# Kernel optimization log

Hardware: AMD Instinct MI355X
Metric: run time of the kernel (lower is better)

The kernel has to match this reference:

```python
import jax, jax.numpy as jnp
import numpy as np

N = 100000   # nodes
E = 800000   # edges
H = 256      # hidden_dim == input_dim
L = 3        # num_layers
G = 64       # graphs in batch


def setup_inputs() -> dict:
    key = jax.random.key(0)
    ks = jax.random.split(key, 16)
    s = 0.05
    inp = {
        'x': jax.random.normal(ks[0], (N, H), jnp.float32),
        'edge_index': jax.random.randint(ks[1], (2, E), 0, N, dtype=jnp.int32),
        'batch': jnp.sort(jax.random.randint(ks[2], (N,), 0, G, dtype=jnp.int32)),
        'Ws': jax.random.normal(ks[3], (L, H, H), jnp.float32) * s,
        'Wn': jax.random.normal(ks[4], (L, H, H), jnp.float32) * s,
        'bs': jnp.zeros((L, H), jnp.float32),
        'att_w': jax.random.normal(ks[5], (H, 1), jnp.float32) * s,
        'att_b': jnp.zeros((1,), jnp.float32),
        'ne_W1': jax.random.normal(ks[6], (H, H // 2), jnp.float32) * s,
        'ne_b1': jnp.zeros((H // 2,), jnp.float32),
        'ne_W2': jax.random.normal(ks[7], (H // 2, 1), jnp.float32) * s,
        'ne_b2': jnp.zeros((1,), jnp.float32),
        'nd_W1': jax.random.normal(ks[8], (H, H // 2), jnp.float32) * s,
        'nd_b1': jnp.zeros((H // 2,), jnp.float32),
        'nd_W2': jax.random.normal(ks[9], (H // 2, 1), jnp.float32) * s,
        'nd_b2': jnp.zeros((1,), jnp.float32),
    }
    return inp


def reference(x, edge_index, batch, Ws, Wn, bs, att_w, att_b,
              ne_W1, ne_b1, ne_W2, ne_b2, nd_W1, nd_b1, nd_W2, nd_b2):
    src, dst = edge_index[0], edge_index[1]
    n = x.shape[0]
    # in-degree for mean aggregation (clamped to avoid div-by-zero)
    deg = jax.ops.segment_sum(jnp.ones(src.shape[0], x.dtype), dst, num_segments=n)
    deg = jnp.maximum(deg, 1.0)[:, None]                    # [N,1]
    # GNN encoder: SAGE-mean layers, ReLU (dropout identity at eval)
    h = x
    for l in range(Ws.shape[0]):
        msg = jax.ops.segment_sum(h[src], dst, num_segments=n) / deg  # [N,H]
        h = jax.nn.relu(h @ Ws[l] + msg @ Wn[l] + bs[l])
    # attention pooling: per-graph softmax over node scores
    s = (h @ att_w + att_b)[:, 0]                           # [N]
    m = jax.ops.segment_max(s, batch, num_segments=G)
    e = jnp.exp(s - m[batch])
    denom = jax.ops.segment_sum(e, batch, num_segments=G)
    alpha = (e / denom[batch])[:, None]                     # [N,1]
    g = jax.ops.segment_sum(alpha * h, batch, num_segments=G)  # [G,H]
    # heads: Linear-ReLU-(Dropout)-Linear
    graph_logits = jax.nn.relu(g @ ne_W1 + ne_b1) @ ne_W2 + ne_b2  # [G,1]
    node_logits = jax.nn.relu(h @ nd_W1 + nd_b1) @ nd_W2 + nd_b2  # [N,1]
    return (graph_logits, node_logits)
```

## Files before the change

kernel.cpp:

```cpp
#include <hip/hip_runtime.h>
#include <hip/hip_bf16.h>

#define HID 256
#define HHALF 128

typedef unsigned short u16;
typedef __attribute__((ext_vector_type(8))) short bf16x8;
typedef __attribute__((ext_vector_type(4))) float f32x4;

__device__ __forceinline__ float bf2f(unsigned int u) {
    unsigned int x = (u & 0xffffu) << 16;
    union { unsigned int i; float f; } c; c.i = x; return c.f;
}
__device__ __forceinline__ float lof(unsigned u) {
    union { unsigned i; float f; } c; c.i = u << 16; return c.f;
}
__device__ __forceinline__ float hif(unsigned u) {
    union { unsigned i; float f; } c; c.i = u & 0xffff0000u; return c.f;
}
__device__ __forceinline__ u16 f2bf(float f) {
    __hip_bfloat16 h = __float2bfloat16(f);
    union { __hip_bfloat16 h; u16 u; } c; c.h = h; return c.u;
}

__device__ __forceinline__ void gload16(const u16* g, u16* l) {
    __builtin_amdgcn_global_load_lds(
        (const __attribute__((address_space(1))) void*)g,
        (__attribute__((address_space(3))) void*)l, 16, 0, 0);
}

__global__ void k_count(const int* __restrict__ dst, int* __restrict__ cnt, int E) {
    int i = blockIdx.x * blockDim.x + threadIdx.x;
    if (i < E) atomicAdd(&cnt[dst[i]], 1);
}

__global__ void k_scan_block(const int* __restrict__ cnt, int* __restrict__ bsum, int n) {
    __shared__ int sd[256];
    int tid = threadIdx.x;
    int i = blockIdx.x * 256 + tid;
    int v = (i < n) ? cnt[i] : 0;
    sd[tid] = v; __syncthreads();
    for (int s = 128; s > 0; s >>= 1) {
        if (tid < s) sd[tid] += sd[tid + s];
        __syncthreads();
    }
    if (tid == 0) bsum[blockIdx.x] = sd[0];
}

__global__ void k_scan_top(int* __restrict__ bsum, int nb) {
    __shared__ int sd[512];
    int t = threadIdx.x;
    int v = (t < nb) ? bsum[t] : 0;
    sd[t] = v; __syncthreads();
    for (int s = 1; s < 512; s <<= 1) {
        int x = (t >= s) ? sd[t - s] : 0;
        __syncthreads();
        sd[t] += x;
        __syncthreads();
    }
    if (t < nb) bsum[t] = sd[t] - v;
}

__global__ void k_scan_down(const int* __restrict__ cnt, const int* __restrict__ boff,
                            int* __restrict__ row_off, int n, int total) {
    __shared__ int sd[256];
    int tid = threadIdx.x;
    int i = blockIdx.x * 256 + tid;
    int v = (i < n) ? cnt[i] : 0;
    sd[tid] = v; __syncthreads();
    for (int s = 1; s < 256; s <<= 1) {
        int x = (tid >= s) ? sd[tid - s] : 0;
        __syncthreads();
        sd[tid] += x;
        __syncthreads();
    }
    if (i < n) row_off[i] = boff[blockIdx.x] + sd[tid] - v;
    if (i == 0) row_off[n] = total;
}

__global__ void k_scatter(const int* __restrict__ src, const int* __restrict__ dst,
                          const int* __restrict__ row_off, int* __restrict__ fill,
                          int* __restrict__ col, int E) {
    int i = blockIdx.x * blockDim.x + threadIdx.x;
    if (i < E) {
        int d = dst[i];
        int p = atomicAdd(&fill[d], 1);
        col[row_off[d] + p] = src[i];
    }
}

__global__ void k_f2b(const float* __restrict__ in, u16* __restrict__ o, int total4) {
    int i = blockIdx.x * blockDim.x + threadIdx.x;
    if (i >= total4) return;
    float4 v = *(const float4*)&in[(size_t)i * 4];
    uint2 p;
    p.x = (unsigned)f2bf(v.x) | ((unsigned)f2bf(v.y) << 16);
    p.y = (unsigned)f2bf(v.z) | ((unsigned)f2bf(v.w) << 16);
    *(uint2*)&o[(size_t)i * 4] = p;
}

__global__ void k_wt_all(const float* __restrict__ Ws, const float* __restrict__ Wn,
                         const float* __restrict__ ndW1,
                         u16* __restrict__ WsT, u16* __restrict__ WnT,
                         u16* __restrict__ ndW1T, int L) {
    int idx = blockIdx.x * 256 + threadIdx.x;
    int mat = idx >> 16;
    int r = idx & 65535;
    int k = r >> 8, c = r & 255;
    if (mat < L) {
        WsT[(size_t)mat * 65536 + c * 256 + k] = f2bf(Ws[(size_t)mat * 65536 + k * 256 + c]);
    } else if (mat < 2 * L) {
        int l = mat - L;
        WnT[(size_t)l * 65536 + c * 256 + k] = f2bf(Wn[(size_t)l * 65536 + k * 256 + c]);
    } else {
        if (c < HHALF) ndW1T[c * 256 + k] = f2bf(ndW1[k * HHALF + c]);
    }
}

__global__ __launch_bounds__(256) void k_agg(
    const u16* __restrict__ h, const int* __restrict__ row_off,
    const int* __restrict__ col, u16* __restrict__ msg, int n) {
    int node = blockIdx.x * 4 + (threadIdx.x >> 6);
    if (node >= n) return;
    int lane = threadIdx.x & 63;
    int half = lane >> 5;
    int t = lane & 31;
    int s0 = row_off[node], s1 = row_off[node + 1];
    float a0 = 0.f, a1 = 0.f, a2 = 0.f, a3 = 0.f;
    float a4 = 0.f, a5 = 0.f, a6 = 0.f, a7 = 0.f;
    int e = s0;
    for (; e + 8 <= s1; e += 8) {
        int c0 = col[e + half];
        int c1 = col[e + 2 + half];
        int c2 = col[e + 4 + half];
        int c3 = col[e + 6 + half];
        uint4 v0 = *(const uint4*)&h[(size_t)c0 * HID + t * 8];
        uint4 v1 = *(const uint4*)&h[(size_t)c1 * HID + t * 8];
        uint4 v2 = *(const uint4*)&h[(size_t)c2 * HID + t * 8];
        uint4 v3 = *(const uint4*)&h[(size_t)c3 * HID + t * 8];
        a0 += (lof(v0.x) + lof(v1.x)) + (lof(v2.x) + lof(v3.x));
        a1 += (hif(v0.x) + hif(v1.x)) + (hif(v2.x) + hif(v3.x));
        a2 += (lof(v0.y) + lof(v1.y)) + (lof(v2.y) + lof(v3.y));
        a3 += (hif(v0.y) + hif(v1.y)) + (hif(v2.y) + hif(v3.y));
        a4 += (lof(v0.z) + lof(v1.z)) + (lof(v2.z) + lof(v3.z));
        a5 += (hif(v0.z) + hif(v1.z)) + (hif(v2.z) + hif(v3.z));
        a6 += (lof(v0.w) + lof(v1.w)) + (lof(v2.w) + lof(v3.w));
        a7 += (hif(v0.w) + hif(v1.w)) + (hif(v2.w) + hif(v3.w));
    }
    if (e < s1) {
        int i0 = e + half, i1 = e + 2 + half, i2 = e + 4 + half, i3 = e + 6 + half;
        float w0 = (i0 < s1) ? 1.f : 0.f; int c0 = col[(i0 < s1) ? i0 : s0];
        float w1 = (i1 < s1) ? 1.f : 0.f; int c1 = col[(i1 < s1) ? i1 : s0];
        float w2 = (i2 < s1) ? 1.f : 0.f; int c2 = col[(i2 < s1) ? i2 : s0];
        float w3 = (i3 < s1) ? 1.f : 0.f; int c3 = col[(i3 < s1) ? i3 : s0];
        uint4 v0 = *(const uint4*)&h[(size_t)c0 * HID + t * 8];
        uint4 v1 = *(const uint4*)&h[(size_t)c1 * HID + t * 8];
        uint4 v2 = *(const uint4*)&h[(size_t)c2 * HID + t * 8];
        uint4 v3 = *(const uint4*)&h[(size_t)c3 * HID + t * 8];
        a0 = fmaf(w0, lof(v0.x), fmaf(w1, lof(v1.x), fmaf(w2, lof(v2.x), fmaf(w3, lof(v3.x), a0))));
        a1 = fmaf(w0, hif(v0.x), fmaf(w1, hif(v1.x), fmaf(w2, hif(v2.x), fmaf(w3, hif(v3.x), a1))));
        a2 = fmaf(w0, lof(v0.y), fmaf(w1, lof(v1.y), fmaf(w2, lof(v2.y), fmaf(w3, lof(v3.y), a2))));
        a3 = fmaf(w0, hif(v0.y), fmaf(w1, hif(v1.y), fmaf(w2, hif(v2.y), fmaf(w3, hif(v3.y), a3))));
        a4 = fmaf(w0, lof(v0.z), fmaf(w1, lof(v1.z), fmaf(w2, lof(v2.z), fmaf(w3, lof(v3.z), a4))));
        a5 = fmaf(w0, hif(v0.z), fmaf(w1, hif(v1.z), fmaf(w2, hif(v2.z), fmaf(w3, hif(v3.z), a5))));
        a6 = fmaf(w0, lof(v0.w), fmaf(w1, lof(v1.w), fmaf(w2, lof(v2.w), fmaf(w3, lof(v3.w), a6))));
        a7 = fmaf(w0, hif(v0.w), fmaf(w1, hif(v1.w), fmaf(w2, hif(v2.w), fmaf(w3, hif(v3.w), a7))));
    }
    a0 += __shfl_xor(a0, 32); a1 += __shfl_xor(a1, 32);
    a2 += __shfl_xor(a2, 32); a3 += __shfl_xor(a3, 32);
    a4 += __shfl_xor(a4, 32); a5 += __shfl_xor(a5, 32);
    a6 += __shfl_xor(a6, 32); a7 += __shfl_xor(a7, 32);
    if (half == 0) {
        int deg = s1 - s0;
        float inv = 1.0f / (float)(deg > 1 ? deg : 1);
        uint4 o;
        o.x = (unsigned)f2bf(a0 * inv) | ((unsigned)f2bf(a1 * inv) << 16);
        o.y = (unsigned)f2bf(a2 * inv) | ((unsigned)f2bf(a3 * inv) << 16);
        o.z = (unsigned)f2bf(a4 * inv) | ((unsigned)f2bf(a5 * inv) << 16);
        o.w = (unsigned)f2bf(a6 * inv) | ((unsigned)f2bf(a7 * inv) << 16);
        *(uint4*)&msg[(size_t)node * HID + t * 8] = o;
    }
}

__global__ __launch_bounds__(512) void k_gemm_bf(
    const u16* __restrict__ A1, const u16* __restrict__ W1t,
    const u16* __restrict__ A2, const u16* __restrict__ W2t,
    const float* __restrict__ bias, u16* __restrict__ out,
    int n, int ncols,
    const float* __restrict__ dotw, const float* __restrict__ dotb,
    float* __restrict__ dotout) {
    __shared__ __align__(16) u16 As[128 * 64];
    __shared__ __align__(16) u16 Bs[256 * 64];
    const int tid  = threadIdx.x;
    const int lane = tid & 63;
    const int w    = tid >> 6;
    const int wr   = w >> 2, wc = w & 3;
    const int brow = blockIdx.x * 128;
    const int nkt  = A2 ? 8 : 4;

    f32x4 acc[4][4];
    #pragma unroll
    for (int m = 0; m < 4; ++m)
        #pragma unroll
        for (int q = 0; q < 4; ++q)
            acc[m][q] = (f32x4){0.f, 0.f, 0.f, 0.f};

    const int as0 = tid, as1 = tid + 512;
    int ar0 = brow + (as0 >> 3); if (ar0 >= n) ar0 = n - 1;
    int ar1 = brow + (as1 >> 3); if (ar1 >= n) ar1 = n - 1;
    const size_t asrc0 = (size_t)ar0 * HID + (size_t)(((as0 & 7) ^ (((as0 >> 3) >> 1) & 7)) * 8);
    const size_t asrc1 = (size_t)ar1 * HID + (size_t)(((as1 & 7) ^ (((as1 >> 3) >> 1) & 7)) * 8);
    u16* adst0 = &As[(w * 64) * 8];
    u16* adst1 = &As[(512 + w * 64) * 8];

    size_t bsrc[4];
    u16*   bdst[4];
    #pragma unroll
    for (int i = 0; i < 4; ++i) {
        int s = tid + i * 512;
        int row = s >> 3;
        bsrc[i] = (size_t)row * HID + (size_t)(((s & 7) ^ ((row >> 1) & 7)) * 8);
        bdst[i] = &Bs[(i * 512 + w * 64) * 8];
    }

    const int lr = lane & 15;
    const int lq = lane >> 4;
    const int swz = (lr >> 1) & 7;

    for (int kt = 0; kt < nkt; ++kt) {
        const u16* A = (kt < 4) ? A1 : A2;
        const u16* W = (kt < 4) ? W1t : W2t;
        const int k0 = (kt & 3) * 64;
        __syncthreads();
        gload16(A + asrc0 + k0, adst0);
        gload16(A + asrc1 + k0, adst1);
        gload16(W + bsrc[0] + k0, bdst[0]);
        gload16(W + bsrc[1] + k0, bdst[1]);
        gload16(W + bsrc[2] + k0, bdst[2]);
        gload16(W + bsrc[3] + k0, bdst[3]);
        __syncthreads();
        #pragma unroll
        for (int ks = 0; ks < 2; ++ks) {
            const int ch = (ks * 4 + lq) ^ swz;
            bf16x8 af[4], bg[4];
            #pragma unroll
            for (int m = 0; m < 4; ++m)
                af[m] = *(const bf16x8*)&As[(wr * 64 + m * 16 + lr) * 64 + ch * 8];
            #pragma unroll
            for (int q = 0; q < 4; ++q)
                bg[q] = *(const bf16x8*)&Bs[(wc * 64 + q * 16 + lr) * 64 + ch * 8];
            #pragma unroll
            for (int m = 0; m < 4; ++m)
                #pragma unroll
                for (int q = 0; q < 4; ++q)
                    acc[m][q] = __builtin_amdgcn_mfma_f32_16x16x32_bf16(
                        bg[q], af[m], acc[m][q], 0, 0, 0);
        }
    }

    #pragma unroll
    for (int m = 0; m < 4; ++m) {
        int row = brow + wr * 64 + m * 16 + lr;
        if (row >= n) continue;
        float dpart = 0.f;
        #pragma unroll
        for (int q = 0; q < 4; ++q) {
            int col = wc * 64 + q * 16 + lq * 4;
            if (col < ncols) {
                float4 bb = *(const float4*)&bias[col];
                float r0 = fmaxf(acc[m][q][0] + bb.x, 0.f);
                float r1 = fmaxf(acc[m][q][1] + bb.y, 0.f);
                float r2 = fmaxf(acc[m][q][2] + bb.z, 0.f);
                float r3 = fmaxf(acc[m][q][3] + bb.w, 0.f);
                if (out) {
                    uint2 o;
                    o.x = (unsigned)f2bf(r0) | ((unsigned)f2bf(r1) << 16);
                    o.y = (unsigned)f2bf(r2) | ((unsigned)f2bf(r3) << 16);
                    *(uint2*)&out[(size_t)row * ncols + col] = o;
                }
                if (dotout) {
                    float4 wv = *(const float4*)&dotw[col];
                    dpart += r0 * wv.x + r1 * wv.y + r2 * wv.z + r3 * wv.w;
                }
            }
        }
        if (dotout && (wc * 64 < ncols)) {
            dpart += __shfl_xor(dpart, 16);
            dpart += __shfl_xor(dpart, 32);
            if (lane < 16) {
                float add = dpart + ((wc == 0) ? dotb[0] : 0.f);
                atomicAdd(&dotout[row], add);
            }
        }
    }
}

__global__ void k_gstart(const int* __restrict__ batch, int* __restrict__ gstart, int n, int G) {
    int i = blockIdx.x * blockDim.x + threadIdx.x;
    if (i >= n) return;
    int b = batch[i];
    int bp = (i == 0) ? -1 : batch[i - 1];
    for (int g = bp + 1; g <= b; ++g) gstart[g] = i;
    if (i == n - 1) {
        for (int g = b + 1; g <= G; ++g) gstart[g] = n;
    }
}

__global__ void k_mdenom(const float* __restrict__ s, const int* __restrict__ gstart,
                         float* __restrict__ m, float* __restrict__ denom) {
    int g = blockIdx.x;
    int t = threadIdx.x;
    int i0 = gstart[g], i1 = gstart[g + 1];
    __shared__ float red[256];
    float mx = -INFINITY;
    for (int i = i0 + t; i < i1; i += 256) mx = fmaxf(mx, s[i]);
    red[t] = mx; __syncthreads();
    for (int st = 128; st; st >>= 1) {
        if (t < st) red[t] = fmaxf(red[t], red[t + st]);
        __syncthreads();
    }
    float gm = red[0];
    __syncthreads();
    float sm = 0.f;
    for (int i = i0 + t; i < i1; i += 256) sm += expf(s[i] - gm);
    red[t] = sm; __syncthreads();
    for (int st = 128; st; st >>= 1) {
        if (t < st) red[t] += red[t + st];
        __syncthreads();
    }
    if (t == 0) { m[g] = gm; denom[g] = red[0]; }
}

__global__ void k_pool(const u16* __restrict__ h, const float* __restrict__ sarr,
                       const float* __restrict__ marr, const float* __restrict__ denom,
                       const int* __restrict__ gstart, float* __restrict__ gpool) {
    int g = blockIdx.x, sp = blockIdx.y, t = threadIdx.x;
    int i0 = gstart[g], i1 = gstart[g + 1];
    int len = i1 - i0;
    int a = i0 + (int)((long long)len * sp / 16);
    int b = i0 + (int)((long long)len * (sp + 1) / 16);
    float dn = denom[g];
    float inv = (dn > 0.f) ? 1.0f / dn : 0.f;
    float mg = marr[g];
    float acc = 0.f;
    for (int i = a; i < b; ++i)
        acc += expf(sarr[i] - mg) * inv * bf2f(h[(size_t)i * HID + t]);
    if (acc != 0.f || sp == 0) atomicAdd(&gpool[g * HID + t], acc);
}

__global__ void k_ghead(const float* __restrict__ gpool, const float* __restrict__ W1,
                        const float* __restrict__ b1, const float* __restrict__ W2,
                        const float* __restrict__ b2, float* __restrict__ out) {
    int g = blockIdx.x, t = threadIdx.x;
    __shared__ float row[HID];
    __shared__ float red[128];
    row[t] = gpool[g * HID + t];
    row[t + 128] = gpool[g * HID + t + 128];
    __syncthreads();
    float acc = 0.f;
    #pragma unroll 8
    for (int k = 0; k < HID; ++k) acc = fmaf(row[k], W1[k * HHALF + t], acc);
    float hid = fmaxf(acc + b1[t], 0.f);
    red[t] = hid * W2[t];
    __syncthreads();
    for (int st = 64; st; st >>= 1) {
        if (t < st) red[t] += red[t + st];
        __syncthreads();
    }
    if (t == 0) out[g] = red[0] + b2[0];
}

extern "C" void kernel_launch(void* const* d_in, const int* in_sizes, int n_in,
                              void* d_out, int out_size, void* d_ws, size_t ws_size,
                              hipStream_t stream) {
    const float* x      = (const float*)d_in[0];
    const int*   eidx   = (const int*)d_in[1];
    const int*   batch  = (const int*)d_in[2];
    const float* Ws     = (const float*)d_in[3];
    const float* Wn     = (const float*)d_in[4];
    const float* bs     = (const float*)d_in[5];
    const float* att_w  = (const float*)d_in[6];
    const float* att_b  = (const float*)d_in[7];
    const float* ne_W1  = (const float*)d_in[8];
    const float* ne_b1  = (const float*)d_in[9];
    const float* ne_W2  = (const float*)d_in[10];
    const float* ne_b2  = (const float*)d_in[11];
    const float* nd_W1  = (const float*)d_in[12];
    const float* nd_b1  = (const float*)d_in[13];
    const float* nd_W2  = (const float*)d_in[14];
    const float* nd_b2  = (const float*)d_in[15];
    float* out = (float*)d_out;

    const int N = in_sizes[2];
    const int E = in_sizes[1] / 2;
    const int L = in_sizes[3] / (HID * HID);
    const int G = out_size - N;

    const int* src = eidx;
    const int* dst = eidx + E;

    size_t off = 0;
    auto alloc = [&](size_t bytes) {
        void* p = (char*)d_ws + off;
        off += (bytes + 255) & ~(size_t)255;
        return p;
    };
    int*   cnt     = (int*)alloc((size_t)N * 4);
    int*   row_off = (int*)alloc((size_t)(N + 1) * 4);
    int*   fill    = (int*)alloc((size_t)N * 4);
    int*   col     = (int*)alloc((size_t)E * 4);
    int*   gstart  = (int*)alloc((size_t)(G + 1) * 4);
    int*   bsum    = (int*)alloc(1024 * 4);
    float* sarr    = (float*)alloc((size_t)N * 4);
    float* marr    = (float*)alloc((size_t)G * 4);
    float* denom   = (float*)alloc((size_t)G * 4);
    float* gpool   = (float*)alloc((size_t)G * HID * 4);
    u16*   xb      = (u16*)alloc((size_t)N * HID * 2);
    u16*   msgb    = (u16*)alloc((size_t)N * HID * 2);
    u16*   hb1     = (u16*)alloc((size_t)N * HID * 2);
    u16*   hb2     = (u16*)alloc((size_t)N * HID * 2);
    u16*   WsT     = (u16*)alloc((size_t)L * HID * HID * 2);
    u16*   WnT     = (u16*)alloc((size_t)L * HID * HID * 2);
    u16*   ndW1T   = (u16*)alloc((size_t)HID * HID * 2);
    (void)ws_size;

    const int eb = (E + 255) / 256;
    const int nb = (N + 255) / 256;

    hipMemsetAsync(cnt, 0, (size_t)N * 4, stream);
    k_count<<<eb, 256, 0, stream>>>(dst, cnt, E);
    k_scan_block<<<nb, 256, 0, stream>>>(cnt, bsum, N);
    k_scan_top<<<1, 512, 0, stream>>>(bsum, nb);
    k_scan_down<<<nb, 256, 0, stream>>>(cnt, bsum, row_off, N, E);
    hipMemsetAsync(fill, 0, (size_t)N * 4, stream);
    k_scatter<<<eb, 256, 0, stream>>>(src, dst, row_off, fill, col, E);

    k_f2b<<<(N * HID / 4 + 255) / 256, 256, 0, stream>>>(x, xb, N * HID / 4);
    k_wt_all<<<(2 * L + 1) * (HID * HID / 256), 256, 0, stream>>>(
        Ws, Wn, nd_W1, WsT, WnT, ndW1T, L);

    hipMemsetAsync(sarr, 0, (size_t)N * 4, stream);
    hipMemsetAsync(out + G, 0, (size_t)N * 4, stream);

    const int gx = (N + 127) / 128;
    const u16* hin = xb;
    u16* hout = hb1;
    for (int l = 0; l < L; ++l) {
        bool last = (l == L - 1);
        k_agg<<<(N + 3) / 4, 256, 0, stream>>>(hin, row_off, col, msgb, N);
        k_gemm_bf<<<gx, 512, 0, stream>>>(
            hin, WsT + (size_t)l * HID * HID, msgb, WnT + (size_t)l * HID * HID,
            bs + (size_t)l * HID, hout, N, HID,
            last ? att_w : nullptr, last ? att_b : nullptr, last ? sarr : nullptr);
        hin = hout;
        hout = (hout == hb1) ? hb2 : hb1;
    }
    const u16* h = hin;

    k_gstart<<<nb, 256, 0, stream>>>(batch, gstart, N, G);
    k_mdenom<<<G, 256, 0, stream>>>(sarr, gstart, marr, denom);
    hipMemsetAsync(gpool, 0, (size_t)G * HID * 4, stream);
    k_pool<<<dim3(G, 16), HID, 0, stream>>>(h, sarr, marr, denom, gstart, gpool);

    k_ghead<<<G, HHALF, 0, stream>>>(gpool, ne_W1, ne_b1, ne_W2, ne_b2, out);

    k_gemm_bf<<<gx, 512, 0, stream>>>(
        h, ndW1T, nullptr, nullptr, nd_b1, nullptr, N, HHALF,
        nd_W2, nd_b2, out + G);
}
```

Measured before the change: 546.3 us.

## Fuse neighbor mean aggregation into the layer GEMM kernel, dropping msg buffer

Replaces the separate aggregation kernel and dual-input GEMM with one per-layer kernel. Each thread gathers a quarter row (64 features) of neighbor sums for one node into 64 fp32 registers, packs them to bf16 and writes them into shared memory as the second half of the K loop. This removes the msg round trip through global memory and one launch per layer. In exchange it adds heavy register pressure (64 accumulators plus 32 packed values alongside the MFMA accumulators in a 512-thread block), lower occupancy, and per-thread serial gathers with weaker memory-level parallelism than the old wave-per-node aggregation.

Result: slower. 675.6 us (+23.7%).

```diff
diff --git a/kernel.cpp b/kernel.cpp
--- a/kernel.cpp
+++ b/kernel.cpp
@@ -117,76 +117,11 @@
     }
 }
 
-__global__ __launch_bounds__(256) void k_agg(
-    const u16* __restrict__ h, const int* __restrict__ row_off,
-    const int* __restrict__ col, u16* __restrict__ msg, int n) {
-    int node = blockIdx.x * 4 + (threadIdx.x >> 6);
-    if (node >= n) return;
-    int lane = threadIdx.x & 63;
-    int half = lane >> 5;
-    int t = lane & 31;
-    int s0 = row_off[node], s1 = row_off[node + 1];
-    float a0 = 0.f, a1 = 0.f, a2 = 0.f, a3 = 0.f;
-    float a4 = 0.f, a5 = 0.f, a6 = 0.f, a7 = 0.f;
-    int e = s0;
-    for (; e + 8 <= s1; e += 8) {
-        int c0 = col[e + half];
-        int c1 = col[e + 2 + half];
-        int c2 = col[e + 4 + half];
-        int c3 = col[e + 6 + half];
-        uint4 v0 = *(const uint4*)&h[(size_t)c0 * HID + t * 8];
-        uint4 v1 = *(const uint4*)&h[(size_t)c1 * HID + t * 8];
-        uint4 v2 = *(const uint4*)&h[(size_t)c2 * HID + t * 8];
-        uint4 v3 = *(const uint4*)&h[(size_t)c3 * HID + t * 8];
-        a0 += (lof(v0.x) + lof(v1.x)) + (lof(v2.x) + lof(v3.x));
-        a1 += (hif(v0.x) + hif(v1.x)) + (hif(v2.x) + hif(v3.x));
-        a2 += (lof(v0.y) + lof(v1.y)) + (lof(v2.y) + lof(v3.y));
-        a3 += (hif(v0.y) + hif(v1.y)) + (hif(v2.y) + hif(v3.y));
-        a4 += (lof(v0.z) + lof(v1.z)) + (lof(v2.z) + lof(v3.z));
-        a5 += (hif(v0.z) + hif(v1.z)) + (hif(v2.z) + hif(v3.z));
-        a6 += (lof(v0.w) + lof(v1.w)) + (lof(v2.w) + lof(v3.w));
-        a7 += (hif(v0.w) + hif(v1.w)) + (hif(v2.w) + hif(v3.w));
-    }
-    if (e < s1) {
-        int i0 = e + half, i1 = e + 2 + half, i2 = e + 4 + half, i3 = e + 6 + half;
-        float w0 = (i0 < s1) ? 1.f : 0.f; int c0 = col[(i0 < s1) ? i0 : s0];
-        float w1 = (i1 < s1) ? 1.f : 0.f; int c1 = col[(i1 < s1) ? i1 : s0];
-        float w2 = (i2 < s1) ? 1.f : 0.f; int c2 = col[(i2 < s1) ? i2 : s0];
-        float w3 = (i3 < s1) ? 1.f : 0.f; int c3 = col[(i3 < s1) ? i3 : s0];
-        uint4 v0 = *(const uint4*)&h[(size_t)c0 * HID + t * 8];
-        uint4 v1 = *(const uint4*)&h[(size_t)c1 * HID + t * 8];
-        uint4 v2 = *(const uint4*)&h[(size_t)c2 * HID + t * 8];
-        uint4 v3 = *(const uint4*)&h[(size_t)c3 * HID + t * 8];
-        a0 = fmaf(w0, lof(v0.x), fmaf(w1, lof(v1.x), fmaf(w2, lof(v2.x), fmaf(w3, lof(v3.x), a0))));
-        a1 = fmaf(w0, hif(v0.x), fmaf(w1, hif(v1.x), fmaf(w2, hif(v2.x), fmaf(w3, hif(v3.x), a1))));
-        a2 = fmaf(w0, lof(v0.y), fmaf(w1, lof(v1.y), fmaf(w2, lof(v2.y), fmaf(w3, lof(v3.y), a2))));
-        a3 = fmaf(w0, hif(v0.y), fmaf(w1, hif(v1.y), fmaf(w2, hif(v2.y), fmaf(w3, hif(v3.y), a3))));
-        a4 = fmaf(w0, lof(v0.z), fmaf(w1, lof(v1.z), fmaf(w2, lof(v2.z), fmaf(w3, lof(v3.z), a4))));
-        a5 = fmaf(w0, hif(v0.z), fmaf(w1, hif(v1.z), fmaf(w2, hif(v2.z), fmaf(w3, hif(v3.z), a5))));
-        a6 = fmaf(w0, lof(v0.w), fmaf(w1, lof(v1.w), fmaf(w2, lof(v2.w), fmaf(w3, lof(v3.w), a6))));
-        a7 = fmaf(w0, hif(v0.w), fmaf(w1, hif(v1.w), fmaf(w2, hif(v2.w), fmaf(w3, hif(v3.w), a7))));
-    }
-    a0 += __shfl_xor(a0, 32); a1 += __shfl_xor(a1, 32);
-    a2 += __shfl_xor(a2, 32); a3 += __shfl_xor(a3, 32);
-    a4 += __shfl_xor(a4, 32); a5 += __shfl_xor(a5, 32);
-    a6 += __shfl_xor(a6, 32); a7 += __shfl_xor(a7, 32);
-    if (half == 0) {
-        int deg = s1 - s0;
-        float inv = 1.0f / (float)(deg > 1 ? deg : 1);
-        uint4 o;
-        o.x = (unsigned)f2bf(a0 * inv) | ((unsigned)f2bf(a1 * inv) << 16);
-        o.y = (unsigned)f2bf(a2 * inv) | ((unsigned)f2bf(a3 * inv) << 16);
-        o.z = (unsigned)f2bf(a4 * inv) | ((unsigned)f2bf(a5 * inv) << 16);
-        o.w = (unsigned)f2bf(a6 * inv) | ((unsigned)f2bf(a7 * inv) << 16);
-        *(uint4*)&msg[(size_t)node * HID + t * 8] = o;
-    }
-}
-
-__global__ __launch_bounds__(512) void k_gemm_bf(
-    const u16* __restrict__ A1, const u16* __restrict__ W1t,
-    const u16* __restrict__ A2, const u16* __restrict__ W2t,
-    const float* __restrict__ bias, u16* __restrict__ out,
-    int n, int ncols,
+__global__ __launch_bounds__(512) void k_layer(
+    const u16* __restrict__ hin, const u16* __restrict__ W1t,
+    const u16* __restrict__ W2t, const float* __restrict__ bias,
+    const int* __restrict__ row_off, const int* __restrict__ colidx,
+    u16* __restrict__ out, int n,
     const float* __restrict__ dotw, const float* __restrict__ dotb,
     float* __restrict__ dotout) {
     __shared__ __align__(16) u16 As[128 * 64];
@@ -196,14 +131,46 @@
     const int w    = tid >> 6;
     const int wr   = w >> 2, wc = w & 3;
     const int brow = blockIdx.x * 128;
-    const int nkt  = A2 ? 8 : 4;
+
+    const int rr = tid >> 2;
+    const int q  = tid & 3;
+    const int grow = brow + rr;
+    float macc[64];
+    #pragma unroll
+    for (int i = 0; i < 64; ++i) macc[i] = 0.f;
+    int deg = 0;
+    if (grow < n) {
+        int s0 = row_off[grow], s1 = row_off[grow + 1];
+        deg = s1 - s0;
+        for (int e = s0; e < s1; ++e) {
+            int c = colidx[e];
+            const u16* hp = hin + (size_t)c * HID + q * 64;
+            #pragma unroll
+            for (int j = 0; j < 8; ++j) {
+                uint4 v = *(const uint4*)(hp + j * 8);
+                macc[j*8+0] += lof(v.x); macc[j*8+1] += hif(v.x);
+                macc[j*8+2] += lof(v.y); macc[j*8+3] += hif(v.y);
+                macc[j*8+4] += lof(v.z); macc[j*8+5] += hif(v.z);
+                macc[j*8+6] += lof(v.w); macc[j*8+7] += hif(v.w);
+            }
+        }
+    }
+    {
+        float inv = 1.0f / (float)(deg > 1 ? deg : 1);
+        #pragma unroll
+        for (int i = 0; i < 64; ++i) macc[i] *= inv;
+    }
+    unsigned mpk[32];
+    #pragma unroll
+    for (int i = 0; i < 32; ++i)
+        mpk[i] = (unsigned)f2bf(macc[2*i]) | ((unsigned)f2bf(macc[2*i+1]) << 16);
 
     f32x4 acc[4][4];
     #pragma unroll
     for (int m = 0; m < 4; ++m)
         #pragma unroll
-        for (int q = 0; q < 4; ++q)
-            acc[m][q] = (f32x4){0.f, 0.f, 0.f, 0.f};
+        for (int p = 0; p < 4; ++p)
+            acc[m][p] = (f32x4){0.f, 0.f, 0.f, 0.f};
 
     const int as0 = tid, as1 = tid + 512;
     int ar0 = brow + (as0 >> 3); if (ar0 >= n) ar0 = n - 1;
@@ -226,14 +193,22 @@
     const int lr = lane & 15;
     const int lq = lane >> 4;
     const int swz = (lr >> 1) & 7;
-
-    for (int kt = 0; kt < nkt; ++kt) {
-        const u16* A = (kt < 4) ? A1 : A2;
+    const int rswz = (rr >> 1) & 7;
+
+    for (int kt = 0; kt < 8; ++kt) {
         const u16* W = (kt < 4) ? W1t : W2t;
         const int k0 = (kt & 3) * 64;
         __syncthreads();
-        gload16(A + asrc0 + k0, adst0);
-        gload16(A + asrc1 + k0, adst1);
+        if (kt < 4) {
+            gload16(hin + asrc0 + k0, adst0);
+            gload16(hin + asrc1 + k0, adst1);
+        } else if (q == (kt & 3)) {
+            #pragma unroll
+            for (int j = 0; j < 8; ++j) {
+                uint4 wv = make_uint4(mpk[j*4+0], mpk[j*4+1], mpk[j*4+2], mpk[j*4+3]);
+                *(uint4*)&As[rr * 64 + ((j ^ rswz) * 8)] = wv;
+            }
+        }
         gload16(W + bsrc[0] + k0, bdst[0]);
         gload16(W + bsrc[1] + k0, bdst[1]);
         gload16(W + bsrc[2] + k0, bdst[2]);
@@ -247,14 +222,14 @@
             for (int m = 0; m < 4; ++m)
                 af[m] = *(const bf16x8*)&As[(wr * 64 + m * 16 + lr) * 64 + ch * 8];
             #pragma unroll
-            for (int q = 0; q < 4; ++q)
-                bg[q] = *(const bf16x8*)&Bs[(wc * 64 + q * 16 + lr) * 64 + ch * 8];
+            for (int p = 0; p < 4; ++p)
+                bg[p] = *(const bf16x8*)&Bs[(wc * 64 + p * 16 + lr) * 64 + ch * 8];
             #pragma unroll
             for (int m = 0; m < 4; ++m)
                 #pragma unroll
-                for (int q = 0; q < 4; ++q)
-                    acc[m][q] = __builtin_amdgcn_mfma_f32_16x16x32_bf16(
-                        bg[q], af[m], acc[m][q], 0, 0, 0);
+                for (int p = 0; p < 4; ++p)
+                    acc[m][p] = __builtin_amdgcn_mfma_f32_16x16x32_bf16(
+                        bg[p], af[m], acc[m][p], 0, 0, 0);
         }
     }
 
@@ -264,27 +239,123 @@
         if (row >= n) continue;
         float dpart = 0.f;
         #pragma unroll
-        for (int q = 0; q < 4; ++q) {
-            int col = wc * 64 + q * 16 + lq * 4;
+        for (int p = 0; p < 4; ++p) {
+            int col = wc * 64 + p * 16 + lq * 4;
+            float4 bb = *(const float4*)&bias[col];
+            float r0 = fmaxf(acc[m][p][0] + bb.x, 0.f);
+            float r1 = fmaxf(acc[m][p][1] + bb.y, 0.f);
+            float r2 = fmaxf(acc[m][p][2] + bb.z, 0.f);
+            float r3 = fmaxf(acc[m][p][3] + bb.w, 0.f);
+            uint2 o;
+            o.x = (unsigned)f2bf(r0) | ((unsigned)f2bf(r1) << 16);
+            o.y = (unsigned)f2bf(r2) | ((unsigned)f2bf(r3) << 16);
+            *(uint2*)&out[(size_t)row * HID + col] = o;
+            if (dotout) {
+                float4 wv = *(const float4*)&dotw[col];
+                dpart += r0 * wv.x + r1 * wv.y + r2 * wv.z + r3 * wv.w;
+            }
+        }
+        if (dotout) {
+            dpart += __shfl_xor(dpart, 16);
+            dpart += __shfl_xor(dpart, 32);
+            if (lane < 16) {
+                float add = dpart + ((wc == 0) ? dotb[0] : 0.f);
+                atomicAdd(&dotout[row], add);
+            }
+        }
+    }
+}
+
+__global__ __launch_bounds__(512) void k_gemm_bf(
+    const u16* __restrict__ A1, const u16* __restrict__ W1t,
+    const float* __restrict__ bias, int n, int ncols,
+    const float* __restrict__ dotw, const float* __restrict__ dotb,
+    float* __restrict__ dotout) {
+    __shared__ __align__(16) u16 As[128 * 64];
+    __shared__ __align__(16) u16 Bs[256 * 64];
+    const int tid  = threadIdx.x;
+    const int lane = tid & 63;
+    const int w    = tid >> 6;
+    const int wr   = w >> 2, wc = w & 3;
+    const int brow = blockIdx.x * 128;
+
+    f32x4 acc[4][4];
+    #pragma unroll
+    for (int m = 0; m < 4; ++m)
+        #pragma unroll
+        for (int p = 0; p < 4; ++p)
+            acc[m][p] = (f32x4){0.f, 0.f, 0.f, 0.f};
+
+    const int as0 = tid, as1 = tid + 512;
+    int ar0 = brow + (as0 >> 3); if (ar0 >= n) ar0 = n - 1;
+    int ar1 = brow + (as1 >> 3); if (ar1 >= n) ar1 = n - 1;
+    const size_t asrc0 = (size_t)ar0 * HID + (size_t)(((as0 & 7) ^ (((as0 >> 3) >> 1) & 7)) * 8);
+    const size_t asrc1 = (size_t)ar1 * HID + (size_t)(((as1 & 7) ^ (((as1 >> 3) >> 1) & 7)) * 8);
+    u16* adst0 = &As[(w * 64) * 8];
+    u16* adst1 = &As[(512 + w * 64) * 8];
+
+    size_t bsrc[4];
+    u16*   bdst[4];
+    #pragma unroll
+    for (int i = 0; i < 4; ++i) {
+        int s = tid + i * 512;
+        int row = s >> 3;
+        bsrc[i] = (size_t)row * HID + (size_t)(((s & 7) ^ ((row >> 1) & 7)) * 8);
+        bdst[i] = &Bs[(i * 512 + w * 64) * 8];
+    }
+
+    const int lr = lane & 15;
+    const int lq = lane >> 4;
+    const int swz = (lr >> 1) & 7;
+
+    for (int kt = 0; kt < 4; ++kt) {
+        const int k0 = kt * 64;
+        __syncthreads();
+        gload16(A1 + asrc0 + k0, adst0);
+        gload16(A1 + asrc1 + k0, adst1);
+        gload16(W1t + bsrc[0] + k0, bdst[0]);
+        gload16(W1t + bsrc[1] + k0, bdst[1]);
+        gload16(W1t + bsrc[2] + k0, bdst[2]);
+        gload16(W1t + bsrc[3] + k0, bdst[3]);
+        __syncthreads();
+        #pragma unroll
+        for (int ks = 0; ks < 2; ++ks) {
+            const int ch = (ks * 4 + lq) ^ swz;
+            bf16x8 af[4], bg[4];
+            #pragma unroll
+            for (int m = 0; m < 4; ++m)
+                af[m] = *(const bf16x8*)&As[(wr * 64 + m * 16 + lr) * 64 + ch * 8];
+            #pragma unroll
+            for (int p = 0; p < 4; ++p)
+                bg[p] = *(const bf16x8*)&Bs[(wc * 64 + p * 16 + lr) * 64 + ch * 8];
+            #pragma unroll
+            for (int m = 0; m < 4; ++m)
+                #pragma unroll
+                for (int p = 0; p < 4; ++p)
+                    acc[m][p] = __builtin_amdgcn_mfma_f32_16x16x32_bf16(
+                        bg[p], af[m], acc[m][p], 0, 0, 0);
+        }
+    }
+
+    #pragma unroll
+    for (int m = 0; m < 4; ++m) {
+        int row = brow + wr * 64 + m * 16 + lr;
+        if (row >= n) continue;
+        float dpart = 0.f;
+        #pragma unroll
+        for (int p = 0; p < 4; ++p) {
+            int col = wc * 64 + p * 16 + lq * 4;
             if (col < ncols) {
                 float4 bb = *(const float4*)&bias[col];
-                float r0 = fmaxf(acc[m][q][0] + bb.x, 0.f);
-                float r1 = fmaxf(acc[m][q][1] + bb.y, 0.f);
-                float r2 = fmaxf(acc[m][q][2] + bb.z, 0.f);
-                float r3 = fmaxf(acc[m][q][3] + bb.w, 0.f);
-                if (out) {
-                    uint2 o;
-                    o.x = (unsigned)f2bf(r0) | ((unsigned)f2bf(r1) << 16);
-                    o.y = (unsigned)f2bf(r2) | ((unsigned)f2bf(r3) << 16);
-                    *(uint2*)&out[(size_t)row * ncols + col] = o;
-                }
-                if (dotout) {
-                    float4 wv = *(const float4*)&dotw[col];
-                    dpart += r0 * wv.x + r1 * wv.y + r2 * wv.z + r3 * wv.w;
-                }
+                float r0 = fmaxf(acc[m][p][0] + bb.x, 0.f);
+                float r1 = fmaxf(acc[m][p][1] + bb.y, 0.f);
+                float r2 = fmaxf(acc[m][p][2] + bb.z, 0.f);
+                float r3 = fmaxf(acc[m][p][3] + bb.w, 0.f);
+                float4 wv = *(const float4*)&dotw[col];
+                dpart += r0 * wv.x + r1 * wv.y + r2 * wv.z + r3 * wv.w;
             }
         }
-        if (dotout && (wc * 64 < ncols)) {
+        if (wc * 64 < ncols) {
             dpart += __shfl_xor(dpart, 16);
             dpart += __shfl_xor(dpart, 32);
             if (lane < 16) {
@@ -416,7 +487,6 @@
     float* denom   = (float*)alloc((size_t)G * 4);
     float* gpool   = (float*)alloc((size_t)G * HID * 4);
     u16*   xb      = (u16*)alloc((size_t)N * HID * 2);
-    u16*   msgb    = (u16*)alloc((size_t)N * HID * 2);
     u16*   hb1     = (u16*)alloc((size_t)N * HID * 2);
     u16*   hb2     = (u16*)alloc((size_t)N * HID * 2);
     u16*   WsT     = (u16*)alloc((size_t)L * HID * HID * 2);
@@ -447,10 +517,9 @@
     u16* hout = hb1;
     for (int l = 0; l < L; ++l) {
         bool last = (l == L - 1);
-        k_agg<<<(N + 3) / 4, 256, 0, stream>>>(hin, row_off, col, msgb, N);
-        k_gemm_bf<<<gx, 512, 0, stream>>>(
-            hin, WsT + (size_t)l * HID * HID, msgb, WnT + (size_t)l * HID * HID,
-            bs + (size_t)l * HID, hout, N, HID,
+        k_layer<<<gx, 512, 0, stream>>>(
+            hin, WsT + (size_t)l * HID * HID, WnT + (size_t)l * HID * HID,
+            bs + (size_t)l * HID, row_off, col, hout, N,
             last ? att_w : nullptr, last ? att_b : nullptr, last ? sarr : nullptr);
         hin = hout;
         hout = (hout == hb1) ? hb2 : hb1;
@@ -465,6 +534,5 @@
     k_ghead<<<G, HHALF, 0, stream>>>(gpool, ne_W1, ne_b1, ne_W2, ne_b2, out);
 
     k_gemm_bf<<<gx, 512, 0, stream>>>(
-        h, ndW1T, nullptr, nullptr, nd_b1, nullptr, N, HHALF,
-        nd_W2, nd_b2, out + G);
-}
+        h, ndW1T, nd_b1, N, HHALF, nd_W2, nd_b2, out + G);
+}
```
